# Kernel optimization log

Hardware: AMD Instinct MI355X
Metric: run time of the kernel (lower is better)

The kernel has to match this reference:

```python
import jax, jax.numpy as jnp
import numpy as np

UP = 4  # upsample factor of DispUpsampleBySlantedPlane


def _l1_warp_cost(fea_l, fea_r, disp):
    """Warp fea_r horizontally by disp (grid_sample bilinear, zeros padding,
    align_corners=True) and return per-pixel L1 distance over channels.
    fea_l, fea_r: [B, C, H, W]; disp: [B, H, W] -> returns [B, H, W]."""
    B, C, H, W = fea_l.shape
    x = jnp.arange(W, dtype=disp.dtype)
    xf = x[None, None, :] - disp              # sample position in right image
    x0 = jnp.floor(xf)
    w1 = xf - x0                              # weight for x0+1
    w0 = 1.0 - w1
    x0i = x0.astype(jnp.int32)
    x1i = x0i + 1
    v0 = ((x0i >= 0) & (x0i < W)).astype(fea_l.dtype)  # zeros padding masks
    v1 = ((x1i >= 0) & (x1i < W)).astype(fea_l.dtype)
    x0c = jnp.clip(x0i, 0, W - 1)
    x1c = jnp.clip(x1i, 0, W - 1)
    idx0 = jnp.broadcast_to(x0c[:, None, :, :], (B, C, H, W))
    idx1 = jnp.broadcast_to(x1c[:, None, :, :], (B, C, H, W))
    g0 = jnp.take_along_axis(fea_r, idx0, axis=3)
    g1 = jnp.take_along_axis(fea_r, idx1, axis=3)
    warped = g0 * (w0 * v0)[:, None] + g1 * (w1 * v1)[:, None]
    return jnp.sum(jnp.abs(fea_l - warped), axis=1)  # L1 over channels


def _tile_warping(tile_plane, fea_l, fea_r):
    B, C, H, W = fea_l.shape
    h, w = tile_plane.shape[2], tile_plane.shape[3]
    d = tile_plane[:, 0]   # [B, h, w]
    dx = tile_plane[:, 1]
    dy = tile_plane[:, 2]
    # slanted-plane offsets for the 4x4 sub-pixels, centered at (UP-1)/2 = 1.5
    off = jnp.arange(UP, dtype=fea_l.dtype) - (UP - 1) / 2.0
    outs = []
    for disp_d in (-1.0, 0.0, 1.0):
        # disp0[b, di, dj, th, tw] = (d + disp_d) + off[di]*dy + off[dj]*dx
        disp0 = ((d + disp_d)[:, None, None]
                 + off[None, :, None, None, None] * dy[:, None, None]
                 + off[None, None, :, None, None] * dx[:, None, None])
        # PixelShuffle(4): full-res disparity [B, H, W]
        disp_full = disp0.transpose(0, 3, 1, 4, 2).reshape(B, H, W)
        cv = _l1_warp_cost(fea_l, fea_r, disp_full)        # [B, H, W]
        # cv[:, :, i::4, j::4] for i,j in 0..3, concatenated on channel dim
        local = cv.reshape(B, h, UP, w, UP).transpose(0, 2, 4, 1, 3)
        outs.append(local.reshape(B, UP * UP, h, w))       # [B, 16, h, w]
    return jnp.concatenate(outs, axis=1)                   # [B, 48, h, w]


def setup_inputs() -> dict:
    key = jax.random.key(0)
    k1, k2, k3 = jax.random.split(key, 3)
    B, C, H, W = 4, 16, 512, 960
    h, w = H // UP, W // UP
    tile_plane = jax.random.normal(k1, (B, 3, h, w), dtype=jnp.float32)
    fea_l = jax.random.normal(k2, (B, C, H, W), dtype=jnp.float32)
    fea_r = jax.random.normal(k3, (B, C, H, W), dtype=jnp.float32)
    return {"tile_plane": tile_plane, "fea_l": fea_l, "fea_r": fea_r}


def reference(tile_plane, fea_l, fea_r):
    return _tile_warping(tile_plane, fea_l, fea_r)
```

## Files before the change

kernel.cpp:

```cpp
#include <hip/hip_runtime.h>


#define UPF 4
#define NB 4
#define NC 16
#define NH 512
#define NW 960
#define TH 128
#define TW 240
#define CHUNK 4
#define LDSROW 992

__global__ __launch_bounds__(256) void tile_warp_kernel(
    const float* __restrict__ tp,
    const float* __restrict__ fl,
    const float* __restrict__ fr,
    float* __restrict__ out)
{
    const int Y = blockIdx.x;
    const int b = blockIdx.y;
    const int t = threadIdx.x;
    const int y = Y >> 2;
    const int i = Y & 3;

    __shared__ float lds[CHUNK * LDSROW];

    float w0v[12], w1v[12], acc[12];
    int   s0[12],  s1[12];

    const bool active = (t < TW);

    if (active) {
        const int tpbase = (b * 3 * TH + y) * TW + t;
        const float d  = tp[tpbase];
        const float dx = tp[tpbase + TH * TW];
        const float dy = tp[tpbase + 2 * TH * TW];
        const float offi = (float)i - 1.5f;
        const float base = d + offi * dy;
#pragma unroll
        for (int k = 0; k < 3; ++k) {
#pragma unroll
            for (int j = 0; j < 4; ++j) {
                const int idx = k * 4 + j;
                const float offj = (float)j - 1.5f;
                const float disp = base + (float)(k - 1) + offj * dx;
                const float xf = (float)(4 * t + j) - disp;
                const float x0f = floorf(xf);
                const float w1 = xf - x0f;
                const float w0 = 1.0f - w1;
                const int x0 = (int)x0f;
                const int x1 = x0 + 1;
                w0v[idx] = (x0 >= 0 && x0 < NW) ? w0 : 0.0f;
                w1v[idx] = (x1 >= 0 && x1 < NW) ? w1 : 0.0f;
                const int x0c = min(max(x0, 0), NW - 1);
                const int x1c = min(max(x1, 0), NW - 1);
                s0[idx] = x0c + (x0c >> 5);
                s1[idx] = x1c + (x1c >> 5);
                acc[idx] = 0.0f;
            }
        }
    }

    for (int c0 = 0; c0 < NC; c0 += CHUNK) {
        __syncthreads();
        if (active) {
#pragma unroll
            for (int cc = 0; cc < CHUNK; ++cc) {
                const float* row = fr + ((size_t)((b * NC + c0 + cc) * NH + Y)) * NW;
                const float4 v = ((const float4*)row)[t];
                const int xb = 4 * t;
                float* l = lds + cc * LDSROW + xb + (xb >> 5);
                l[0] = v.x; l[1] = v.y; l[2] = v.z; l[3] = v.w;
            }
        }
        __syncthreads();
        if (active) {
#pragma unroll
            for (int cc = 0; cc < CHUNK; ++cc) {
                const float* lrow = fl + ((size_t)((b * NC + c0 + cc) * NH + Y)) * NW;
                const float4 fv = ((const float4*)lrow)[t];
                const float flv[4] = {fv.x, fv.y, fv.z, fv.w};
                const float* __restrict__ L = lds + cc * LDSROW;
#pragma unroll
                for (int k = 0; k < 3; ++k) {
#pragma unroll
                    for (int j = 0; j < 4; ++j) {
                        const int idx = k * 4 + j;
                        const float g0 = L[s0[idx]];
                        const float g1 = L[s1[idx]];
                        const float wv = g0 * w0v[idx] + g1 * w1v[idx];
                        acc[idx] += fabsf(flv[j] - wv);
                    }
                }
            }
        }
    }

    if (active) {
#pragma unroll
        for (int k = 0; k < 3; ++k) {
#pragma unroll
            for (int j = 0; j < 4; ++j) {
                const int ch = k * 16 + i * 4 + j;
                out[((size_t)(b * 48 + ch) * TH + y) * TW + t] = acc[k * 4 + j];
            }
        }
    }
}

extern "C" void kernel_launch(void* const* d_in, const int* in_sizes, int n_in,
                              void* d_out, int out_size, void* d_ws, size_t ws_size,
                              hipStream_t stream) {
    const float* tp = (const float*)d_in[0];
    const float* fl = (const float*)d_in[1];
    const float* fr = (const float*)d_in[2];
    float* out = (float*)d_out;

    dim3 grid(NH, NB);
    dim3 block(256);
    tile_warp_kernel<<<grid, block, 0, stream>>>(tp, fl, fr, out);
}
```

Measured before the change: 274.2 us.

## Use one thread per pixel with async global-to-LDS double-buffered staging

After: 272.1 us. Within noise of the previous version (-0.8%).

```diff
diff --git a/kernel.cpp b/kernel.cpp
--- a/kernel.cpp
+++ b/kernel.cpp
@@ -1,111 +1,119 @@
 #include <hip/hip_runtime.h>
 
 
-#define UPF 4
 #define NB 4
 #define NC 16
 #define NH 512
 #define NW 960
 #define TH 128
 #define TW 240
-#define CHUNK 4
-#define LDSROW 992
+#define HW (NH * NW)
+#define GUARD 16
+#define CHUNK 8
+#define CBUF (2 * GUARD + CHUNK * NW)
 
-__global__ __launch_bounds__(256) void tile_warp_kernel(
+typedef const __attribute__((address_space(1))) unsigned int* gas_u32;
+typedef __attribute__((address_space(3))) unsigned int* las_u32;
+
+__device__ __forceinline__ void stage16(const float* g, float* l) {
+    __builtin_amdgcn_global_load_lds((gas_u32)g, (las_u32)l, 16, 0, 0);
+}
+
+__global__ __launch_bounds__(960, 8) void tile_warp_kernel(
     const float* __restrict__ tp,
     const float* __restrict__ fl,
     const float* __restrict__ fr,
     float* __restrict__ out)
 {
+    const int u = threadIdx.x;
     const int Y = blockIdx.x;
     const int b = blockIdx.y;
-    const int t = threadIdx.x;
-    const int y = Y >> 2;
-    const int i = Y & 3;
+    const int y = Y >> 2, i = Y & 3;
+    const int T = u >> 2, j = u & 3;
 
-    __shared__ float lds[CHUNK * LDSROW];
+    __shared__ float smem[2][CBUF];
 
-    float w0v[12], w1v[12], acc[12];
-    int   s0[12],  s1[12];
+    const float* frrow = fr + (size_t)(b * NC) * HW + (size_t)Y * NW;
+    const float* flrow = fl + (size_t)(b * NC) * HW + (size_t)Y * NW + u;
 
-    const bool active = (t < TW);
+    {
+        const int s0 = u, s1 = u + 960;
+        stage16(frrow + (s0 / 240) * HW + 4 * (s0 % 240), &smem[0][GUARD + 4 * s0]);
+        stage16(frrow + (s1 / 240) * HW + 4 * (s1 % 240), &smem[0][GUARD + 4 * s1]);
+    }
 
-    if (active) {
-        const int tpbase = (b * 3 * TH + y) * TW + t;
-        const float d  = tp[tpbase];
-        const float dx = tp[tpbase + TH * TW];
-        const float dy = tp[tpbase + 2 * TH * TW];
-        const float offi = (float)i - 1.5f;
-        const float base = d + offi * dy;
+    const int tpb = (b * 3 * TH + y) * TW + T;
+    const float d   = tp[tpb];
+    const float dxv = tp[tpb + TH * TW];
+    const float dyv = tp[tpb + 2 * TH * TW];
+    const float base = d + ((float)i - 1.5f) * dyv + ((float)j - 1.5f) * dxv;
+    const float xf  = (float)u - base;
+    const float x0f = floorf(xf);
+    const float w1  = xf - x0f;
+    const float w0  = 1.0f - w1;
+    const int   x0  = (int)x0f;
+    const int   p   = x0 - 1;
+    const int   p_cl = max(min(p, NW + 12), -GUARD);
+
+    float w0k[3], w1k[3];
 #pragma unroll
-        for (int k = 0; k < 3; ++k) {
+    for (int kk = 0; kk < 3; ++kk) {
+        const int xa = p + 2 - kk;
+        const int xb = p + 3 - kk;
+        w0k[kk] = (xa >= 0 && xa < NW) ? w0 : 0.0f;
+        w1k[kk] = (xb >= 0 && xb < NW) ? w1 : 0.0f;
+    }
+    float acc0 = 0.f, acc1 = 0.f, acc2 = 0.f;
+
+    __syncthreads();
+
+    {
+        const float* frrow1 = frrow + CHUNK * HW;
+        const int s0 = u, s1 = u + 960;
+        stage16(frrow1 + (s0 / 240) * HW + 4 * (s0 % 240), &smem[1][GUARD + 4 * s0]);
+        stage16(frrow1 + (s1 / 240) * HW + 4 * (s1 % 240), &smem[1][GUARD + 4 * s1]);
+    }
+
+    {
+        float flv[CHUNK];
 #pragma unroll
-            for (int j = 0; j < 4; ++j) {
-                const int idx = k * 4 + j;
-                const float offj = (float)j - 1.5f;
-                const float disp = base + (float)(k - 1) + offj * dx;
-                const float xf = (float)(4 * t + j) - disp;
-                const float x0f = floorf(xf);
-                const float w1 = xf - x0f;
-                const float w0 = 1.0f - w1;
-                const int x0 = (int)x0f;
-                const int x1 = x0 + 1;
-                w0v[idx] = (x0 >= 0 && x0 < NW) ? w0 : 0.0f;
-                w1v[idx] = (x1 >= 0 && x1 < NW) ? w1 : 0.0f;
-                const int x0c = min(max(x0, 0), NW - 1);
-                const int x1c = min(max(x1, 0), NW - 1);
-                s0[idx] = x0c + (x0c >> 5);
-                s1[idx] = x1c + (x1c >> 5);
-                acc[idx] = 0.0f;
-            }
+        for (int c = 0; c < CHUNK; ++c) flv[c] = flrow[c * HW];
+#pragma unroll
+        for (int c = 0; c < CHUNK; ++c) {
+            const float* L = &smem[0][GUARD + c * NW + p_cl];
+            const float m0 = L[0], m1 = L[1], m2 = L[2], m3 = L[3];
+            const float wv0 = m2 * w0k[0] + m3 * w1k[0];
+            const float wv1 = m1 * w0k[1] + m2 * w1k[1];
+            const float wv2 = m0 * w0k[2] + m1 * w1k[2];
+            acc0 += fabsf(flv[c] - wv0);
+            acc1 += fabsf(flv[c] - wv1);
+            acc2 += fabsf(flv[c] - wv2);
         }
     }
 
-    for (int c0 = 0; c0 < NC; c0 += CHUNK) {
-        __syncthreads();
-        if (active) {
+    __syncthreads();
+
+    {
+        float flv[CHUNK];
 #pragma unroll
-            for (int cc = 0; cc < CHUNK; ++cc) {
-                const float* row = fr + ((size_t)((b * NC + c0 + cc) * NH + Y)) * NW;
-                const float4 v = ((const float4*)row)[t];
-                const int xb = 4 * t;
-                float* l = lds + cc * LDSROW + xb + (xb >> 5);
-                l[0] = v.x; l[1] = v.y; l[2] = v.z; l[3] = v.w;
-            }
-        }
-        __syncthreads();
-        if (active) {
+        for (int c = 0; c < CHUNK; ++c) flv[c] = flrow[(CHUNK + c) * HW];
 #pragma unroll
-            for (int cc = 0; cc < CHUNK; ++cc) {
-                const float* lrow = fl + ((size_t)((b * NC + c0 + cc) * NH + Y)) * NW;
-                const float4 fv = ((const float4*)lrow)[t];
-                const float flv[4] = {fv.x, fv.y, fv.z, fv.w};
-                const float* __restrict__ L = lds + cc * LDSROW;
-#pragma unroll
-                for (int k = 0; k < 3; ++k) {
-#pragma unroll
-                    for (int j = 0; j < 4; ++j) {
-                        const int idx = k * 4 + j;
-                        const float g0 = L[s0[idx]];
-                        const float g1 = L[s1[idx]];
-                        const float wv = g0 * w0v[idx] + g1 * w1v[idx];
-                        acc[idx] += fabsf(flv[j] - wv);
-                    }
-                }
-            }
+        for (int c = 0; c < CHUNK; ++c) {
+            const float* L = &smem[1][GUARD + c * NW + p_cl];
+            const float m0 = L[0], m1 = L[1], m2 = L[2], m3 = L[3];
+            const float wv0 = m2 * w0k[0] + m3 * w1k[0];
+            const float wv1 = m1 * w0k[1] + m2 * w1k[1];
+            const float wv2 = m0 * w0k[2] + m1 * w1k[2];
+            acc0 += fabsf(flv[c] - wv0);
+            acc1 += fabsf(flv[c] - wv1);
+            acc2 += fabsf(flv[c] - wv2);
         }
     }
 
-    if (active) {
-#pragma unroll
-        for (int k = 0; k < 3; ++k) {
-#pragma unroll
-            for (int j = 0; j < 4; ++j) {
-                const int ch = k * 16 + i * 4 + j;
-                out[((size_t)(b * 48 + ch) * TH + y) * TW + t] = acc[k * 4 + j];
-            }
-        }
-    }
+    const size_t obase = ((size_t)(b * 48 + i * 4 + j) * TH + y) * TW + T;
+    out[obase]                        = acc0;
+    out[obase + 16 * (size_t)TH * TW] = acc1;
+    out[obase + 32 * (size_t)TH * TW] = acc2;
 }
 
 extern "C" void kernel_launch(void* const* d_in, const int* in_sizes, int n_in,
@@ -117,6 +125,6 @@
     float* out = (float*)d_out;
 
     dim3 grid(NH, NB);
-    dim3 block(256);
+    dim3 block(960);
     tile_warp_kernel<<<grid, block, 0, stream>>>(tp, fl, fr, out);
 }
```
